# Optimization experiments

Measured on AMD Instinct MI355X. Metric: run time of the kernel, lower is better.

The kernel has to match this reference:

```python
import jax, jax.numpy as jnp
import numpy as np

KS = 3      # kernel_size
PAD = 1     # zero padding applied to x before sampling
STRIDE = 1  # stride of p_conv and final conv (as written in the repo)


def conv2d(x, w, b=None, stride=1, padding=0):
    out = jax.lax.conv_general_dilated(
        x, w, (stride, stride), [(padding, padding), (padding, padding)],
        dimension_numbers=("NCHW", "OIHW", "NCHW"))
    if b is not None:
        out = out + b[None, :, None, None]
    return out


def setup_inputs() -> dict:
    key = jax.random.key(0)
    k1, k2, k3, k4 = jax.random.split(key, 4)
    bsz, inc, outc, H, W = 4, 64, 128, 128, 128
    N = KS * KS
    x = jax.random.normal(k1, (bsz, inc, H, W), dtype=jnp.float32)
    # p_conv: Conv2d(inc, 2*ks*ks, 3, padding=1) with bias (small weights -> modest offsets)
    w_p = jax.random.normal(k2, (2 * N, inc, 3, 3), dtype=jnp.float32) * 0.02
    b_p = jax.random.normal(k3, (2 * N,), dtype=jnp.float32) * 0.1
    # final conv: Conv2d(inc, outc, ks, stride=stride, bias=None)
    w_conv = jax.random.normal(k4, (outc, inc, KS, KS), dtype=jnp.float32) * 0.05
    return {"x": x, "w_p": w_p, "b_p": b_p, "w_conv": w_conv}


def deform_conv_forward(x, w_p, b_p, w_conv):
    ks, pad, stride = KS, PAD, STRIDE
    offset = conv2d(x, w_p, b_p, stride=stride, padding=1)  # (b, 2N, oh, ow)
    N = offset.shape[1] // 2
    bsz, c, _, _ = x.shape
    oh, ow = offset.shape[2], offset.shape[3]
    xp = jnp.pad(x, ((0, 0), (0, 0), (pad, pad), (pad, pad)))
    Hp, Wp = xp.shape[2], xp.shape[3]

    # p_n: kernel-grid offsets, order matches torch.meshgrid 'ij' then flatten
    r = jnp.arange(-(ks - 1) // 2, (ks - 1) // 2 + 1, dtype=x.dtype)
    pnx, pny = jnp.meshgrid(r, r, indexing="ij")
    p_n = jnp.concatenate([pnx.ravel(), pny.ravel()])[None, :, None, None]  # (1,2N,1,1)

    # p_0: base sampling coordinates (1-indexed into padded image)
    i0 = jnp.arange(1, oh * stride + 1, stride, dtype=x.dtype)
    j0 = jnp.arange(1, ow * stride + 1, stride, dtype=x.dtype)
    p0x = jnp.broadcast_to(i0[:, None], (oh, ow))[None, None]
    p0y = jnp.broadcast_to(j0[None, :], (oh, ow))[None, None]
    p_0 = jnp.concatenate([jnp.tile(p0x, (1, N, 1, 1)), jnp.tile(p0y, (1, N, 1, 1))], axis=1)

    p = (p_0 + p_n + offset).transpose(0, 2, 3, 1)  # (b, oh, ow, 2N)

    q_lt_f = jnp.floor(p)
    q_rb_f = q_lt_f + 1.0

    def clamp_q(q):
        return jnp.concatenate(
            [jnp.clip(q[..., :N], 0, Hp - 1), jnp.clip(q[..., N:], 0, Wp - 1)],
            axis=-1).astype(jnp.int32)

    q_lt = clamp_q(q_lt_f)
    q_rb = clamp_q(q_rb_f)
    q_lb = jnp.concatenate([q_lt[..., :N], q_rb[..., N:]], axis=-1)
    q_rt = jnp.concatenate([q_rb[..., :N], q_lt[..., N:]], axis=-1)

    # clamp p itself (indices are detached in torch; gradients flow only through p here)
    p = jnp.concatenate(
        [jnp.clip(p[..., :N], 0, Hp - 1), jnp.clip(p[..., N:], 0, Wp - 1)], axis=-1)
    px, py = p[..., :N], p[..., N:]

    qf = lambda q: q.astype(x.dtype)
    g_lt = (1 + (qf(q_lt[..., :N]) - px)) * (1 + (qf(q_lt[..., N:]) - py))
    g_rb = (1 - (qf(q_rb[..., :N]) - px)) * (1 - (qf(q_rb[..., N:]) - py))
    g_lb = (1 + (qf(q_lb[..., :N]) - px)) * (1 - (qf(q_lb[..., N:]) - py))
    g_rt = (1 - (qf(q_rt[..., :N]) - px)) * (1 + (qf(q_rt[..., N:]) - py))

    x_flat = xp.reshape(bsz, c, Hp * Wp)

    def get_x_q(q):
        idx = q[..., :N] * Wp + q[..., N:]                     # (b, oh, ow, N)
        idxf = jnp.broadcast_to(idx.reshape(bsz, 1, -1), (bsz, c, oh * ow * N))
        return jnp.take_along_axis(x_flat, idxf, axis=2).reshape(bsz, c, oh, ow, N)

    x_off = (g_lt[:, None] * get_x_q(q_lt) + g_rb[:, None] * get_x_q(q_rb)
             + g_lb[:, None] * get_x_q(q_lb) + g_rt[:, None] * get_x_q(q_rt))

    # _reshape_x_offset: (b,c,oh,ow,ks*ks) -> (b,c,oh*ks,ow*ks)
    x_off = x_off.reshape(bsz, c, oh, ow, ks, ks).transpose(0, 1, 2, 4, 3, 5)
    x_off = x_off.reshape(bsz, c, oh * ks, ow * ks)

    return conv2d(x_off, w_conv, None, stride=stride, padding=0)


def reference(x, w_p, b_p, w_conv):
    return deform_conv_forward(x, w_p, b_p, w_conv)
```

## Files before the change

### kernel.cpp

```cpp
#include <hip/hip_runtime.h>
#include <hip/hip_bf16.h>

#define B_   4
#define IC   64
#define OC   128
#define HH   128
#define WW   128
#define HP   130
#define XOF  384
#define XPAD 388
#define OH2  382

typedef __attribute__((ext_vector_type(4))) float f32x4;
typedef __attribute__((ext_vector_type(8))) __bf16 bf16x8;
typedef __attribute__((ext_vector_type(8))) unsigned short us8;
typedef __attribute__((ext_vector_type(4), aligned(4))) float f32x4u;

__device__ __forceinline__ void gload16(const void* gsrc, void* ldst) {
    __builtin_amdgcn_global_load_lds(
        (const __attribute__((address_space(1))) void*)gsrc,
        (__attribute__((address_space(3))) void*)ldst, 16, 0, 0);
}

__global__ __launch_bounds__(256) void nchw2nhwc(const float* __restrict__ x,
                                                 float* __restrict__ xt) {
    __shared__ float tile[64][33];
    int bid = blockIdx.x;
    int xt4 = bid & 3;
    int y   = (bid >> 2) & 127;
    int b   = bid >> 9;
    int x0  = xt4 * 32;

    int t  = threadIdx.x;
    int xl = t & 31;
    int c8 = t >> 5;
#pragma unroll
    for (int it = 0; it < 8; ++it) {
        int c = it * 8 + c8;
        tile[c][xl] = x[(((size_t)b * IC + c) * HH + y) * WW + x0 + xl];
    }
    __syncthreads();
    int c  = t & 63;
    int xw = t >> 6;
#pragma unroll
    for (int it = 0; it < 8; ++it) {
        int xx = it * 4 + xw;
        xt[(((size_t)b * HH + y) * WW + x0 + xx) * IC + c] = tile[c][xx];
    }
}

__global__ __launch_bounds__(256) void offset_lds4(const float* __restrict__ x,
                                                   const float* __restrict__ w_p,
                                                   const float* __restrict__ b_p,
                                                   float* __restrict__ off) {
    __shared__ float part[4][64][18];

    int t   = threadIdx.x;
    int pxl = t & 63;
    int icq = t >> 6;
    int seg = blockIdx.x & 1;
    int row = blockIdx.x >> 1;
    int py  = row & 127;
    int b   = row >> 7;
    int px  = seg * 64 + pxl;
    int ic0 = __builtin_amdgcn_readfirstlane(icq << 4);

    float acc[18];
#pragma unroll
    for (int co = 0; co < 18; ++co) acc[co] = 0.f;

    const float* xb = x + ((size_t)b * IC + ic0) * HH * WW;

    for (int ci = 0; ci < 16; ++ci) {
        const float* xc = xb + (size_t)ci * HH * WW;
        float xv[9];
#pragma unroll
        for (int ky = 0; ky < 3; ++ky) {
            int yy = py + ky - 1;
            bool yok = (yy >= 0) && (yy < HH);
#pragma unroll
            for (int kx = 0; kx < 3; ++kx) {
                int xx = px + kx - 1;
                bool ok = yok && (xx >= 0) && (xx < WW);
                xv[ky * 3 + kx] = ok ? xc[yy * WW + xx] : 0.f;
            }
        }
#pragma unroll
        for (int co = 0; co < 18; ++co) {
            const float* wrow = w_p + ((size_t)co * IC + ic0 + ci) * 9;
            f32x4u w0 = *(const f32x4u*)wrow;
            f32x4u w1 = *(const f32x4u*)(wrow + 4);
            float  w8 = wrow[8];
            acc[co] = fmaf(w0.x, xv[0], acc[co]);
            acc[co] = fmaf(w0.y, xv[1], acc[co]);
            acc[co] = fmaf(w0.z, xv[2], acc[co]);
            acc[co] = fmaf(w0.w, xv[3], acc[co]);
            acc[co] = fmaf(w1.x, xv[4], acc[co]);
            acc[co] = fmaf(w1.y, xv[5], acc[co]);
            acc[co] = fmaf(w1.z, xv[6], acc[co]);
            acc[co] = fmaf(w1.w, xv[7], acc[co]);
            acc[co] = fmaf(w8,   xv[8], acc[co]);
        }
    }

#pragma unroll
    for (int co = 0; co < 18; ++co) part[icq][pxl][co] = acc[co];
    __syncthreads();

    for (int co = icq; co < 18; co += 4) {
        float s = b_p[co] + part[0][pxl][co] + part[1][pxl][co]
                          + part[2][pxl][co] + part[3][pxl][co];
        off[((size_t)b * 18 + co) * HH * WW + (size_t)py * WW + px] = s;
    }
}

__global__ __launch_bounds__(256) void prep_w(const float* __restrict__ wc,
                                              unsigned short* __restrict__ Bt) {
    int t = blockIdx.x * 256 + threadIdx.x;
    if (t >= 18 * 4 * 128 * 8) return;
    int e  = t & 7;
    int oc = (t >> 3) & 127;
    int kg = (t >> 10) & 3;
    int s  = t >> 12;
    int ic = ((s & 1) << 5) + (kg << 3) + e;
    int kpos = s >> 1;
    int ky = kpos / 3, kx = kpos % 3;
    float v = wc[(((size_t)oc * IC + ic) * 3 + ky) * 3 + kx];
    __hip_bfloat16 h = __float2bfloat16(v);
    Bt[t] = reinterpret_cast<unsigned short&>(h);
}

__global__ __launch_bounds__(256) void sample_nhwc(const float* __restrict__ xt,
                                                   const float* __restrict__ off,
                                                   unsigned short* __restrict__ xoff,
                                                   int b0, int nwg) {
    int orig = blockIdx.x;
    int chunk = nwg >> 3;
    int wg = (orig & 7) * chunk + (orig >> 3);

    int xtile = wg % 12;
    int tmp = wg / 12;
    int yy  = tmp % XOF;
    int bl  = tmp / XOF;
    int b   = b0 + bl;
    int xx0 = xtile * 32;

    int t  = threadIdx.x;
    int xl = t & 31;
    int cg = t >> 5;
    int xx = xx0 + xl;

    int j = xx / 3, kw = xx % 3;
    int i = yy / 3, kh = yy % 3;
    int n = kh * 3 + kw;

    const float* offb = off + (size_t)b * 18 * HH * WW + (size_t)i * WW + j;
    float offr = offb[(size_t)n * HH * WW];
    float offc = offb[(size_t)(n + 9) * HH * WW];

    float pr = (float)(i + kh) + offr;
    float pc = (float)(j + kw) + offc;

    float r0f = floorf(pr), c0f = floorf(pc);
    int r0 = min(max((int)r0f, 0), HP - 1);
    int c0 = min(max((int)c0f, 0), HP - 1);
    int r1 = min(max((int)(r0f + 1.f), 0), HP - 1);
    int c1 = min(max((int)(c0f + 1.f), 0), HP - 1);

    float prc = fminf(fmaxf(pr, 0.f), (float)(HP - 1));
    float pcc = fminf(fmaxf(pc, 0.f), (float)(HP - 1));

    float R0 = 1.f + ((float)r0 - prc);
    float R1 = 1.f - ((float)r1 - prc);
    float C0 = 1.f + ((float)c0 - pcc);
    float C1 = 1.f - ((float)c1 - pcc);

    int rr0 = r0 - 1, cc0 = c0 - 1, rr1 = r1 - 1, cc1 = c1 - 1;
    if (!(rr0 >= 0 && rr0 < HH)) R0 = 0.f;
    if (!(rr1 >= 0 && rr1 < HH)) R1 = 0.f;
    float C0m = (cc0 >= 0 && cc0 < WW) ? C0 : 0.f;
    float C1m = (cc1 >= 0 && cc1 < WW) ? C1 : 0.f;
    int ra0 = min(max(rr0, 0), HH - 1);
    int ra1 = min(max(rr1, 0), HH - 1);
    int ca0 = min(max(cc0, 0), WW - 1);
    int ca1 = min(max(cc1, 0), WW - 1);

    const float* xb = xt + (size_t)b * HH * WW * IC + cg * 8;
    const float* p00 = xb + ((size_t)ra0 * WW + ca0) * IC;
    const float* p01 = xb + ((size_t)ra0 * WW + ca1) * IC;
    const float* p10 = xb + ((size_t)ra1 * WW + ca0) * IC;
    const float* p11 = xb + ((size_t)ra1 * WW + ca1) * IC;

    us8 res;
#pragma unroll
    for (int h = 0; h < 2; ++h) {
        f32x4u a  = *(const f32x4u*)(p00 + h * 4);
        f32x4u bb = *(const f32x4u*)(p01 + h * 4);
        f32x4u cc = *(const f32x4u*)(p10 + h * 4);
        f32x4u dd = *(const f32x4u*)(p11 + h * 4);
#pragma unroll
        for (int e = 0; e < 4; ++e) {
            float v = R0 * (C0m * a[e] + C1m * bb[e]) +
                      R1 * (C0m * cc[e] + C1m * dd[e]);
            __hip_bfloat16 hh = __float2bfloat16(v);
            res[h * 4 + e] = reinterpret_cast<unsigned short&>(hh);
        }
    }

    size_t di = ((((size_t)bl * XOF + yy) * 8 + cg) * XPAD + xx) * 8;
    *(us8*)(xoff + di) = res;
}

__global__ __launch_bounds__(256) void conv2_mfma(const unsigned short* __restrict__ xoff,
                                                  const unsigned short* __restrict__ Bt,
                                                  float* __restrict__ out,
                                                  int b0, int nwg) {
    __shared__ __align__(16) char lds[24576];

    int orig = blockIdx.x;
    int q = nwg >> 3, r = nwg & 7;
    int xcd = orig & 7, loc = orig >> 3;
    int wgid = (xcd < r ? xcd * (q + 1) : r * (q + 1) + (xcd - r) * q) + loc;

    int xt  = wgid % 3;
    int tmp = wgid / 3;
    int oy  = tmp % OH2;
    int bl  = tmp / OH2;
    int x0  = xt << 7;

    int tid  = threadIdx.x;
    int wave = tid >> 6, lane = tid & 63;
    int wm = wave >> 1;
    int wn = wave & 1;
    int lr = lane & 15, lc = lane >> 4;

    const char* xb = (const char*)xoff + (size_t)bl * ((size_t)XOF * 8 * XPAD * 16);
    const char* bt = (const char*)Bt;
    const int boff = ((lc * 128) + wn * 64 + lr) * 16;

    f32x4 acc[4][4];
#pragma unroll
    for (int mf = 0; mf < 4; ++mf)
#pragma unroll
        for (int nf = 0; nf < 4; ++nf)
            acc[mf][nf] = (f32x4){0.f, 0.f, 0.f, 0.f};

    auto stageA_full = [&](int abuf, int s6) {
        int ky  = s6 >> 1;
        int ich = s6 & 1;
#pragma unroll
        for (int qq = 0; qq < 3; ++qq) {
            int L  = wave * 3 + qq;
            int cg = L / 3, seg = L % 3;
            const char* src = xb +
                (((size_t)(oy + ky) * 8 + ich * 4 + cg) * XPAD + x0 + seg * 64 + lane) * 16;
            char* dst = lds + abuf * 12288 + (cg * 192 + seg * 64) * 16;
            gload16(src, dst);
        }
    };

    auto loadB = [&](bf16x8* dst, int t) {
        int s6 = t / 3, kx = t % 3;
        int sB = ((s6 >> 1) * 3 + kx) * 2 + (s6 & 1);
        const char* bsrc = bt + (size_t)sB * 8192 + boff;
#pragma unroll
        for (int nf = 0; nf < 4; ++nf)
            dst[nf] = *(const bf16x8*)(bsrc + nf * 256);
    };

    bf16x8 bcur[4], bnxt[4];

    stageA_full(0, 0);
    loadB(bcur, 0);
    __syncthreads();

    int abuf = 0;
    for (int s6 = 0; s6 < 6; ++s6) {
#pragma unroll
        for (int kx = 0; kx < 3; ++kx) {
            int t = s6 * 3 + kx;
            if (t + 1 < 18) loadB(bnxt, t + 1);
            if (kx == 0 && s6 + 1 < 6) stageA_full(abuf ^ 1, s6 + 1);

            const char* abase = lds + abuf * 12288;
            bf16x8 af[4];
#pragma unroll
            for (int mf = 0; mf < 4; ++mf)
                af[mf] = *(const bf16x8*)(abase +
                    (lc * 192 + wm * 64 + mf * 16 + lr + kx) * 16);
#pragma unroll
            for (int mf = 0; mf < 4; ++mf)
#pragma unroll
                for (int nf = 0; nf < 4; ++nf)
                    acc[mf][nf] = __builtin_amdgcn_mfma_f32_16x16x32_bf16(
                        af[mf], bcur[nf], acc[mf][nf], 0, 0, 0);
#pragma unroll
            for (int nf = 0; nf < 4; ++nf) bcur[nf] = bnxt[nf];
        }
        if (s6 + 1 < 6) {
            __syncthreads();
            abuf ^= 1;
        }
    }

    int b = b0 + bl;
#pragma unroll
    for (int mf = 0; mf < 4; ++mf) {
        int ox0 = x0 + wm * 64 + mf * 16 + (lc << 2);
#pragma unroll
        for (int nf = 0; nf < 4; ++nf) {
            int oc = wn * 64 + nf * 16 + lr;
            float* po = out + (((size_t)b * OC + oc) * OH2 + oy) * OH2 + ox0;
            if (ox0 + 3 < OH2) {
                *(f32x4u*)po = acc[mf][nf];
            } else {
#pragma unroll
                for (int rr = 0; rr < 4; ++rr)
                    if (ox0 + rr < OH2) po[rr] = acc[mf][nf][rr];
            }
        }
    }
}

extern "C" void kernel_launch(void* const* d_in, const int* in_sizes, int n_in,
                              void* d_out, int out_size, void* d_ws, size_t ws_size,
                              hipStream_t stream) {
    const float* x      = (const float*)d_in[0];
    const float* w_p    = (const float*)d_in[1];
    const float* b_p    = (const float*)d_in[2];
    const float* w_conv = (const float*)d_in[3];
    float* out = (float*)d_out;

    const size_t offElems = (size_t)B_ * 18 * HH * WW;
    const size_t xtElems  = (size_t)B_ * HH * WW * IC;
    const size_t btElems  = (size_t)18 * 4 * 128 * 8;
    const size_t xofElems = (size_t)XOF * 8 * XPAD * 8;
    const size_t slack    = 16384;

    float* off = (float*)d_ws;
    float* xtb = off + offElems;
    unsigned short* Bt   = (unsigned short*)(xtb + xtElems);
    unsigned short* xoff = Bt + btElems;

    const size_t headBytes = (offElems + xtElems) * 4 + btElems * 2;
    const bool allBatch = ws_size >= headBytes + 4 * xofElems * 2 + slack;

    prep_w<<<(int)((btElems + 255) / 256), 256, 0, stream>>>(w_conv, Bt);
    nchw2nhwc<<<2048, 256, 0, stream>>>(x, xtb);
    offset_lds4<<<1024, 256, 0, stream>>>(x, w_p, b_p, off);

    if (allBatch) {
        int snwg = 12 * XOF * B_;
        sample_nhwc<<<snwg, 256, 0, stream>>>(xtb, off, xoff, 0, snwg);
        int cnwg = 3 * OH2 * B_;
        conv2_mfma<<<cnwg, 256, 0, stream>>>(xoff, Bt, out, 0, cnwg);
    } else {
        for (int b = 0; b < B_; ++b) {
            int snwg = 12 * XOF;
            sample_nhwc<<<snwg, 256, 0, stream>>>(xtb, off, xoff, b, snwg);
            int cnwg = 3 * OH2;
            conv2_mfma<<<cnwg, 256, 0, stream>>>(xoff, Bt, out, b, cnwg);
        }
    }
}
```

Before: 249.1 us.

## Give each wave private LDS A-tiles to drop block-wide barriers in conv2 MFMA

```diff
diff --git a/kernel.cpp b/kernel.cpp
--- a/kernel.cpp
+++ b/kernel.cpp
@@ -215,7 +215,7 @@
                                                   const unsigned short* __restrict__ Bt,
                                                   float* __restrict__ out,
                                                   int b0, int nwg) {
-    __shared__ __align__(16) char lds[24576];
+    __shared__ __align__(16) char lds[65536];
 
     int orig = blockIdx.x;
     int q = nwg >> 3, r = nwg & 7;
@@ -237,6 +237,7 @@
     const char* xb = (const char*)xoff + (size_t)bl * ((size_t)XOF * 8 * XPAD * 16);
     const char* bt = (const char*)Bt;
     const int boff = ((lc * 128) + wn * 64 + lr) * 16;
+    char* waveLds = lds + wave * 16384;
 
     f32x4 acc[4][4];
 #pragma unroll
@@ -245,18 +246,18 @@
         for (int nf = 0; nf < 4; ++nf)
             acc[mf][nf] = (f32x4){0.f, 0.f, 0.f, 0.f};
 
-    auto stageA_full = [&](int abuf, int s6) {
+    auto stageA = [&](int abuf, int s6) {
         int ky  = s6 >> 1;
         int ich = s6 & 1;
 #pragma unroll
-        for (int qq = 0; qq < 3; ++qq) {
-            int L  = wave * 3 + qq;
-            int cg = L / 3, seg = L % 3;
-            const char* src = xb +
-                (((size_t)(oy + ky) * 8 + ich * 4 + cg) * XPAD + x0 + seg * 64 + lane) * 16;
-            char* dst = lds + abuf * 12288 + (cg * 192 + seg * 64) * 16;
-            gload16(src, dst);
-        }
+        for (int cg = 0; cg < 4; ++cg)
+#pragma unroll
+            for (int seg = 0; seg < 2; ++seg) {
+                const char* src = xb +
+                    (((size_t)(oy + ky) * 8 + ich * 4 + cg) * XPAD +
+                     x0 + wm * 64 + seg * 64 + lane) * 16;
+                gload16(src, waveLds + abuf * 8192 + (cg * 2 + seg) * 1024);
+            }
     };
 
     auto loadB = [&](bf16x8* dst, int t) {
@@ -270,24 +271,23 @@
 
     bf16x8 bcur[4], bnxt[4];
 
-    stageA_full(0, 0);
+    stageA(0, 0);
     loadB(bcur, 0);
-    __syncthreads();
 
     int abuf = 0;
     for (int s6 = 0; s6 < 6; ++s6) {
+        asm volatile("s_waitcnt vmcnt(0)" ::: "memory");
+        __builtin_amdgcn_sched_barrier(0);
+        if (s6 + 1 < 6) stageA(abuf ^ 1, s6 + 1);
 #pragma unroll
         for (int kx = 0; kx < 3; ++kx) {
             int t = s6 * 3 + kx;
             if (t + 1 < 18) loadB(bnxt, t + 1);
-            if (kx == 0 && s6 + 1 < 6) stageA_full(abuf ^ 1, s6 + 1);
-
-            const char* abase = lds + abuf * 12288;
+            const char* abase = waveLds + abuf * 8192;
             bf16x8 af[4];
 #pragma unroll
             for (int mf = 0; mf < 4; ++mf)
-                af[mf] = *(const bf16x8*)(abase +
-                    (lc * 192 + wm * 64 + mf * 16 + lr + kx) * 16);
+                af[mf] = *(const bf16x8*)(abase + lc * 2048 + (mf * 16 + lr + kx) * 16);
 #pragma unroll
             for (int mf = 0; mf < 4; ++mf)
 #pragma unroll
@@ -297,10 +297,7 @@
 #pragma unroll
             for (int nf = 0; nf < 4; ++nf) bcur[nf] = bnxt[nf];
         }
-        if (s6 + 1 < 6) {
-            __syncthreads();
-            abuf ^= 1;
-        }
+        abuf ^= 1;
     }
 
     int b = b0 + bl;
```

After: 264.5 us. 6.2% more time.

## Stage weight tiles through LDS with async loads and split A staging

Applied to the files above, without the earlier changes.

```diff
diff --git a/kernel.cpp b/kernel.cpp
--- a/kernel.cpp
+++ b/kernel.cpp
@@ -21,6 +21,8 @@
         (const __attribute__((address_space(1))) void*)gsrc,
         (__attribute__((address_space(3))) void*)ldst, 16, 0, 0);
 }
+
+#define WAITV(N) asm volatile("s_waitcnt vmcnt(" #N ")" ::: "memory")
 
 __global__ __launch_bounds__(256) void nchw2nhwc(const float* __restrict__ x,
                                                  float* __restrict__ xt) {
@@ -215,7 +217,7 @@
                                                   const unsigned short* __restrict__ Bt,
                                                   float* __restrict__ out,
                                                   int b0, int nwg) {
-    __shared__ __align__(16) char lds[24576];
+    __shared__ __align__(16) char lds[40960];
 
     int orig = blockIdx.x;
     int q = nwg >> 3, r = nwg & 7;
@@ -236,7 +238,6 @@
 
     const char* xb = (const char*)xoff + (size_t)bl * ((size_t)XOF * 8 * XPAD * 16);
     const char* bt = (const char*)Bt;
-    const int boff = ((lc * 128) + wn * 64 + lr) * 16;
 
     f32x4 acc[4][4];
 #pragma unroll
@@ -245,62 +246,83 @@
         for (int nf = 0; nf < 4; ++nf)
             acc[mf][nf] = (f32x4){0.f, 0.f, 0.f, 0.f};
 
-    auto stageA_full = [&](int abuf, int s6) {
+    auto stageA = [&](int abuf, int s6, int third) {
         int ky  = s6 >> 1;
         int ich = s6 & 1;
+        int L   = third * 4 + wave;
+        int cg  = L / 3, seg = L % 3;
+        const char* src = xb +
+            (((size_t)(oy + ky) * 8 + ich * 4 + cg) * XPAD + x0 + seg * 64 + lane) * 16;
+        char* dst = lds + abuf * 12288 + (cg * 192 + seg * 64) * 16;
+        gload16(src, dst);
+    };
+    auto stageA_full = [&](int abuf, int s6) {
 #pragma unroll
         for (int qq = 0; qq < 3; ++qq) {
-            int L  = wave * 3 + qq;
-            int cg = L / 3, seg = L % 3;
+            int ky  = s6 >> 1;
+            int ich = s6 & 1;
+            int L   = wave * 3 + qq;
+            int cg  = L / 3, seg = L % 3;
             const char* src = xb +
                 (((size_t)(oy + ky) * 8 + ich * 4 + cg) * XPAD + x0 + seg * 64 + lane) * 16;
             char* dst = lds + abuf * 12288 + (cg * 192 + seg * 64) * 16;
             gload16(src, dst);
         }
     };
-
-    auto loadB = [&](bf16x8* dst, int t) {
+    auto stageB = [&](int bbuf, int t) {
         int s6 = t / 3, kx = t % 3;
         int sB = ((s6 >> 1) * 3 + kx) * 2 + (s6 & 1);
-        const char* bsrc = bt + (size_t)sB * 8192 + boff;
+        const char* bsrc = bt + (size_t)sB * 8192;
+#pragma unroll
+        for (int g2 = 0; g2 < 2; ++g2) {
+            int g = wave * 2 + g2;
+            gload16(bsrc + (size_t)g * 1024 + lane * 16,
+                    lds + 24576 + bbuf * 8192 + g * 1024);
+        }
+    };
+
+    auto compute = [&](int abuf, int bbuf, int kx) {
+        const char* abase = lds + abuf * 12288;
+        const char* bbase = lds + 24576 + bbuf * 8192;
+        bf16x8 af[4], bfr[4];
+#pragma unroll
+        for (int mf = 0; mf < 4; ++mf)
+            af[mf] = *(const bf16x8*)(abase +
+                (lc * 192 + wm * 64 + mf * 16 + lr + kx) * 16);
 #pragma unroll
         for (int nf = 0; nf < 4; ++nf)
-            dst[nf] = *(const bf16x8*)(bsrc + nf * 256);
+            bfr[nf] = *(const bf16x8*)(bbase +
+                (lc * 128 + wn * 64 + nf * 16 + lr) * 16);
+#pragma unroll
+        for (int mf = 0; mf < 4; ++mf)
+#pragma unroll
+            for (int nf = 0; nf < 4; ++nf)
+                acc[mf][nf] = __builtin_amdgcn_mfma_f32_16x16x32_bf16(
+                    af[mf], bfr[nf], acc[mf][nf], 0, 0, 0);
     };
 
-    bf16x8 bcur[4], bnxt[4];
-
     stageA_full(0, 0);
-    loadB(bcur, 0);
-    __syncthreads();
-
-    int abuf = 0;
+    stageB(0, 0);
+
+    int abuf = 0, bbuf = 0;
+#pragma unroll
     for (int s6 = 0; s6 < 6; ++s6) {
 #pragma unroll
         for (int kx = 0; kx < 3; ++kx) {
-            int t = s6 * 3 + kx;
-            if (t + 1 < 18) loadB(bnxt, t + 1);
-            if (kx == 0 && s6 + 1 < 6) stageA_full(abuf ^ 1, s6 + 1);
-
-            const char* abase = lds + abuf * 12288;
-            bf16x8 af[4];
-#pragma unroll
-            for (int mf = 0; mf < 4; ++mf)
-                af[mf] = *(const bf16x8*)(abase +
-                    (lc * 192 + wm * 64 + mf * 16 + lr + kx) * 16);
-#pragma unroll
-            for (int mf = 0; mf < 4; ++mf)
-#pragma unroll
-                for (int nf = 0; nf < 4; ++nf)
-                    acc[mf][nf] = __builtin_amdgcn_mfma_f32_16x16x32_bf16(
-                        af[mf], bcur[nf], acc[mf][nf], 0, 0, 0);
-#pragma unroll
-            for (int nf = 0; nf < 4; ++nf) bcur[nf] = bnxt[nf];
-        }
-        if (s6 + 1 < 6) {
-            __syncthreads();
-            abuf ^= 1;
-        }
+            const int t = s6 * 3 + kx;
+            if (t + 1 < 18) stageB(bbuf ^ 1, t + 1);
+            if (s6 + 1 < 6) stageA(abuf ^ 1, s6 + 1, kx);
+            if (s6 < 5)          { WAITV(3); }
+            else if (kx < 2)     { WAITV(2); }
+            else                 { WAITV(0); }
+            __builtin_amdgcn_s_barrier();
+            __builtin_amdgcn_sched_barrier(0);
+            compute(abuf, bbuf, kx);
+            __builtin_amdgcn_sched_barrier(0);
+            __builtin_amdgcn_s_barrier();
+            bbuf ^= 1;
+        }
+        abuf ^= 1;
     }
 
     int b = b0 + bl;
```

New measurement: 249.3 us. About the same (+0.1%).
